# Performance work log

Measured on AMD Instinct MI355X. Metric: run time of the kernel, lower is better.

The kernel has to match this reference:

```python
import jax, jax.numpy as jnp
import numpy as np

N = 64000
B = 16
F_IN = 16
N_PROP = 64
N_DIM = 4
K = 40        # n_neighbours
F_OUT = 128


def setup_inputs() -> dict:
    key = jax.random.key(0)
    ks = jax.random.split(key, 8)
    x = jax.random.normal(ks[0], (N, F_IN), dtype=jnp.float32)
    row_splits = (jnp.arange(B + 1, dtype=jnp.int32) * (N // B))
    # Dense params (glorot-ish scaling)
    Ws = jax.random.normal(ks[1], (F_IN, N_DIM), dtype=jnp.float32) / jnp.sqrt(F_IN)
    bs = jnp.zeros((N_DIM,), dtype=jnp.float32)
    Wf = jax.random.normal(ks[2], (F_IN, N_PROP), dtype=jnp.float32) / jnp.sqrt(F_IN)
    bf = jnp.zeros((N_PROP,), dtype=jnp.float32)
    n_in = F_IN + 2 * N_PROP  # x concat [max, mean]
    Wo = jax.random.normal(ks[3], (n_in, F_OUT), dtype=jnp.float32) / jnp.sqrt(n_in)
    bo = jnp.zeros((F_OUT,), dtype=jnp.float32)
    return {"x": x, "row_splits": row_splits, "Ws": Ws, "bs": bs,
            "Wf": Wf, "bf": bf, "Wo": Wo, "bo": bo}


def _knn_indices(coords, n_per_seg, n_seg, k):
    # coords: [N, D] with equal-size segments of n_per_seg nodes.
    c = coords.reshape(n_seg, n_per_seg, -1)              # [B, n, D]
    nn = jnp.sum(c * c, axis=-1)                          # [B, n]
    d2 = nn[:, :, None] + nn[:, None, :] - 2.0 * jnp.einsum('bnd,bmd->bnm', c, c)
    _, idx_local = jax.lax.top_k(-d2, k + 1)              # sorted by distance, self first
    idx_local = idx_local[:, :, 1:]                       # drop self -> [B, n, K]
    offsets = (jnp.arange(n_seg, dtype=idx_local.dtype) * n_per_seg)[:, None, None]
    return (idx_local + offsets).reshape(n_seg * n_per_seg, k)  # global [N, K]


def reference(x, row_splits, Ws, bs, Wf, bf, Wo, bo):
    n_seg = row_splits.shape[0] - 1
    n_per_seg = x.shape[0] // n_seg

    coords = x @ Ws + bs                                  # [N, D]
    feat = x @ Wf + bf                                    # [N, P]

    idx = _knn_indices(coords, n_per_seg, n_seg, K)       # [N, K]
    simple_distance = coords[:, None, :] - coords[idx]    # [N, K, D]
    rot_distance = jnp.sum(simple_distance ** 2, axis=-1) # [N, K]
    # gauss_of_lin(x) = exp(-|x|)
    weights = jnp.exp(-jnp.abs(rot_distance * 10.0 + 1e-5))[..., None]  # [N, K, 1]

    neighbour_features = feat[idx]                        # [N, K, P] gather
    wnf = neighbour_features * weights
    collected = jnp.concatenate([jnp.max(wnf, axis=1), jnp.mean(wnf, axis=1)], axis=-1)
    features = jnp.concatenate([x, collected], axis=-1)   # [N, F_IN + 2P]
    return jnp.tanh(features @ Wo + bo)                   # [N, F_OUT]
```

## Files before the change

### kernel.cpp

```cpp
#include <hip/hip_runtime.h>
#include <math.h>

#define NTOT   64000
#define NSEG   16
#define SEGSZ  4000
#define KNN    40
#define FIN    16
#define NPROP  64
#define FOUT   128
#define NIN    144


__global__ __launch_bounds__(256)
void k1_proj(const float* __restrict__ x,
             const float* __restrict__ Ws, const float* __restrict__ bs,
             const float* __restrict__ Wf, const float* __restrict__ bf,
             float4* __restrict__ coords, float* __restrict__ nn,
             float* __restrict__ feat, float* __restrict__ features)
{
    __shared__ float sWs[FIN * 4];
    __shared__ float sbs[4];
    __shared__ float sWf[FIN * NPROP];
    __shared__ float sbf[NPROP];
    int t = threadIdx.x;
    if (t < FIN * 4) sWs[t] = Ws[t];
    if (t < 4) sbs[t] = bs[t];
    for (int i = t; i < FIN * NPROP; i += 256) sWf[i] = Wf[i];
    if (t < NPROP) sbf[t] = bf[t];
    __syncthreads();

    int q = blockIdx.x * 256 + t;
    const float4* xv = (const float4*)(x + q * FIN);
    float4 x0 = xv[0], x1 = xv[1], x2 = xv[2], x3 = xv[3];
    float xr[FIN] = {x0.x, x0.y, x0.z, x0.w, x1.x, x1.y, x1.z, x1.w,
                     x2.x, x2.y, x2.z, x2.w, x3.x, x3.y, x3.z, x3.w};

    float c0 = sbs[0], c1 = sbs[1], c2 = sbs[2], c3 = sbs[3];
#pragma unroll
    for (int k = 0; k < FIN; k++) {
        float xk = xr[k];
        c0 += xk * sWs[k * 4 + 0];
        c1 += xk * sWs[k * 4 + 1];
        c2 += xk * sWs[k * 4 + 2];
        c3 += xk * sWs[k * 4 + 3];
    }
    coords[q] = make_float4(c0, c1, c2, c3);
    nn[q] = c0 * c0 + c1 * c1 + c2 * c2 + c3 * c3;

    float4* frow = (float4*)(features + q * NIN);
    frow[0] = x0; frow[1] = x1; frow[2] = x2; frow[3] = x3;

#pragma unroll
    for (int f0 = 0; f0 < NPROP; f0 += 4) {
        float a0 = sbf[f0], a1 = sbf[f0 + 1], a2 = sbf[f0 + 2], a3 = sbf[f0 + 3];
#pragma unroll
        for (int k = 0; k < FIN; k++) {
            float xk = xr[k];
            const float* w = &sWf[k * NPROP + f0];
            a0 += xk * w[0]; a1 += xk * w[1]; a2 += xk * w[2]; a3 += xk * w[3];
        }
        *(float4*)(feat + q * NPROP + f0) = make_float4(a0, a1, a2, a3);
    }
}

#define K2_WPB 4
#define QPW    2

__device__ __forceinline__ void ce(unsigned int& a, unsigned int& b)
{
    unsigned int lo = min(a, b);
    unsigned int hi = max(a, b);
    a = lo; b = hi;
}

__device__ __forceinline__ void batch4(unsigned int (&arr)[4],
                                       unsigned int k0, unsigned int k1,
                                       unsigned int k2, unsigned int k3)
{
    ce(k0, k1); ce(k2, k3); ce(k0, k2); ce(k1, k3); ce(k1, k2);
    arr[0] = min(arr[0], k3);
    arr[1] = min(arr[1], k2);
    arr[2] = min(arr[2], k1);
    arr[3] = min(arr[3], k0);
    ce(arr[0], arr[2]); ce(arr[1], arr[3]); ce(arr[0], arr[1]); ce(arr[2], arr[3]);
}

__global__ __launch_bounds__(256)
void k2_knn_agg(const float4* __restrict__ coords, const float* __restrict__ nn,
                const float* __restrict__ feat, float* __restrict__ features)
{
    __shared__ unsigned int win[K2_WPB][QPW][KNN];
    int lane = threadIdx.x & 63;
    int wave = threadIdx.x >> 6;
    int qA = (blockIdx.x * K2_WPB + wave) * QPW;
    int seg = qA / SEGSZ;
    int segbase = seg * SEGSZ;
    int lqA = qA - segbase;
    float4 qcA = coords[qA];
    float4 qcB = coords[qA + 1];
    const float4* cbase = coords + segbase;
    const float* nbase = nn + segbase;

    float sqqA = qcA.x * qcA.x + qcA.y * qcA.y + qcA.z * qcA.z + qcA.w * qcA.w;
    float sqqB = qcB.x * qcB.x + qcB.y * qcB.y + qcB.z * qcB.z + qcB.w * qcB.w;
    float mAx = -2.f * qcA.x, mAy = -2.f * qcA.y, mAz = -2.f * qcA.z, mAw = -2.f * qcA.w;
    float mBx = -2.f * qcB.x, mBy = -2.f * qcB.y, mBz = -2.f * qcB.z, mBw = -2.f * qcB.w;

    unsigned int arrA[4], arrB[4];
#pragma unroll
    for (int n = 0; n < 4; n++) { arrA[n] = 0xFFFFFFFFu; arrB[n] = 0xFFFFFFFFu; }

#define DKEY(cc, njs, j, mx, my, mz, mw) \
    ((__float_as_uint(fmaxf(fmaf((cc).x, (mx), fmaf((cc).y, (my), \
      fmaf((cc).z, (mz), fmaf((cc).w, (mw), (njs))))), 0.f)) & 0xFFFFF000u) \
     | (unsigned int)(j))

    for (int b = 0; b < 15; b++) {
        int j0 = b * 256 + lane;
        float4 c0 = cbase[j0];
        float4 c1 = cbase[j0 + 64];
        float4 c2 = cbase[j0 + 128];
        float4 c3 = cbase[j0 + 192];
        float n0 = nbase[j0], n1 = nbase[j0 + 64];
        float n2 = nbase[j0 + 128], n3 = nbase[j0 + 192];
        unsigned int a0 = DKEY(c0, n0 + sqqA, j0,       mAx, mAy, mAz, mAw);
        unsigned int a1 = DKEY(c1, n1 + sqqA, j0 + 64,  mAx, mAy, mAz, mAw);
        unsigned int a2 = DKEY(c2, n2 + sqqA, j0 + 128, mAx, mAy, mAz, mAw);
        unsigned int a3 = DKEY(c3, n3 + sqqA, j0 + 192, mAx, mAy, mAz, mAw);
        batch4(arrA, a0, a1, a2, a3);
        unsigned int b0 = DKEY(c0, n0 + sqqB, j0,       mBx, mBy, mBz, mBw);
        unsigned int b1 = DKEY(c1, n1 + sqqB, j0 + 64,  mBx, mBy, mBz, mBw);
        unsigned int b2 = DKEY(c2, n2 + sqqB, j0 + 128, mBx, mBy, mBz, mBw);
        unsigned int b3 = DKEY(c3, n3 + sqqB, j0 + 192, mBx, mBy, mBz, mBw);
        batch4(arrB, b0, b1, b2, b3);
    }
    {
        int j0 = 3840 + lane;
        float4 c0 = cbase[j0];
        float4 c1 = cbase[j0 + 64];
        float n0 = nbase[j0], n1 = nbase[j0 + 64];
        int j2 = j0 + 128;
        int j2c = (j2 < SEGSZ) ? j2 : (SEGSZ - 1);
        float4 c2 = cbase[j2c];
        float n2 = nbase[j2c];
        unsigned int a0 = DKEY(c0, n0 + sqqA, j0,      mAx, mAy, mAz, mAw);
        unsigned int a1 = DKEY(c1, n1 + sqqA, j0 + 64, mAx, mAy, mAz, mAw);
        unsigned int a2 = (j2 < SEGSZ)
            ? (unsigned int)DKEY(c2, n2 + sqqA, j2, mAx, mAy, mAz, mAw)
            : 0xFFFFFFFFu;
        batch4(arrA, a0, a1, a2, 0xFFFFFFFFu);
        unsigned int b0 = DKEY(c0, n0 + sqqB, j0,      mBx, mBy, mBz, mBw);
        unsigned int b1 = DKEY(c1, n1 + sqqB, j0 + 64, mBx, mBy, mBz, mBw);
        unsigned int b2 = (j2 < SEGSZ)
            ? (unsigned int)DKEY(c2, n2 + sqqB, j2, mBx, mBy, mBz, mBw)
            : 0xFFFFFFFFu;
        batch4(arrB, b0, b1, b2, 0xFFFFFFFFu);
    }
#undef DKEY

    const float* fseg = feat + segbase * NPROP + lane;

#define SELECT_AND_AGG(ARR, LQ, Q, SLOT)                                      \
    {                                                                         \
        unsigned int klo = 0u, khi = 0xFFFFFFFFu;                             \
        for (int it = 0; it < 32; it++) {                                     \
            unsigned int mid = klo + ((khi - klo) >> 1);                      \
            int c = 0;                                                        \
            c += __popcll(__ballot(ARR[0] <= mid));                           \
            c += __popcll(__ballot(ARR[1] <= mid));                           \
            c += __popcll(__ballot(ARR[2] <= mid));                           \
            c += __popcll(__ballot(ARR[3] <= mid));                           \
            if (c >= KNN + 1) khi = mid; else klo = mid + 1;                  \
        }                                                                     \
        unsigned int K41 = khi;                                               \
        int base = 0;                                                         \
        _Pragma("unroll")                                                     \
        for (int n = 0; n < 4; n++) {                                         \
            bool qual = (ARR[n] <= K41) &&                                    \
                        ((ARR[n] & 0xFFFu) != (unsigned int)(LQ));            \
            unsigned long long m = __ballot(qual);                            \
            int pos = base + __builtin_amdgcn_mbcnt_hi((unsigned int)(m >> 32),\
                            __builtin_amdgcn_mbcnt_lo((unsigned int)m, 0));   \
            if (qual && pos < KNN) win[wave][SLOT][pos] = ARR[n];             \
            base += __popcll(m);                                              \
            if (base >= KNN) break;                                           \
        }                                                                     \
        float mxv = -INFINITY, smv = 0.f;                                     \
        _Pragma("unroll 4")                                                   \
        for (int k = 0; k < KNN; k++) {                                       \
            unsigned int key = win[wave][SLOT][k];                            \
            float d2 = __uint_as_float(key & 0xFFFFF000u);                    \
            int nl = (int)(key & 0xFFFu);                                     \
            float w = __expf(-(d2 * 10.f + 1e-5f));                           \
            float f = fseg[nl * NPROP];                                       \
            float wf = w * f;                                                 \
            mxv = fmaxf(mxv, wf);                                             \
            smv += wf;                                                        \
        }                                                                     \
        features[(Q) * NIN + FIN + lane]         = mxv;                       \
        features[(Q) * NIN + FIN + NPROP + lane] = smv * (1.f / KNN);         \
    }

    SELECT_AND_AGG(arrA, lqA,     qA,     0)
    SELECT_AND_AGG(arrB, lqA + 1, qA + 1, 1)
#undef SELECT_AND_AGG
}

__global__ __launch_bounds__(256)
void k4_gemm(const float* __restrict__ features, const float* __restrict__ Wo,
             const float* __restrict__ bo, float* __restrict__ out)
{
    __shared__ float As[16 * 128];
    __shared__ float Bs[16 * 128];
    int t = threadIdx.x;
    int ty = t >> 4, tx = t & 15;
    int r0 = blockIdx.x * 128;

    float acc[8][8];
#pragma unroll
    for (int i = 0; i < 8; i++)
#pragma unroll
        for (int j = 0; j < 8; j++) acc[i][j] = 0.f;

    int arow = t >> 1;
    int acol = (t & 1) * 8;

    for (int c = 0; c < 9; c++) {
        const float* asrc = features + (r0 + arow) * NIN + c * 16 + acol;
        float4 a0 = *(const float4*)(asrc);
        float4 a1 = *(const float4*)(asrc + 4);
        const float4* bsrc = (const float4*)(Wo + c * 2048 + t * 8);
        float4 b0 = bsrc[0], b1 = bsrc[1];
        As[(acol + 0) * 128 + arow] = a0.x;
        As[(acol + 1) * 128 + arow] = a0.y;
        As[(acol + 2) * 128 + arow] = a0.z;
        As[(acol + 3) * 128 + arow] = a0.w;
        As[(acol + 4) * 128 + arow] = a1.x;
        As[(acol + 5) * 128 + arow] = a1.y;
        As[(acol + 6) * 128 + arow] = a1.z;
        As[(acol + 7) * 128 + arow] = a1.w;
        *(float4*)&Bs[t * 8]     = b0;
        *(float4*)&Bs[t * 8 + 4] = b1;
        __syncthreads();
#pragma unroll
        for (int kk = 0; kk < 16; kk++) {
            float4 av0 = *(float4*)&As[kk * 128 + ty * 8];
            float4 av1 = *(float4*)&As[kk * 128 + ty * 8 + 4];
            float4 bv0 = *(float4*)&Bs[kk * 128 + tx * 8];
            float4 bv1 = *(float4*)&Bs[kk * 128 + tx * 8 + 4];
            float a[8] = {av0.x, av0.y, av0.z, av0.w, av1.x, av1.y, av1.z, av1.w};
            float b[8] = {bv0.x, bv0.y, bv0.z, bv0.w, bv1.x, bv1.y, bv1.z, bv1.w};
#pragma unroll
            for (int i = 0; i < 8; i++)
#pragma unroll
                for (int j = 0; j < 8; j++) acc[i][j] += a[i] * b[j];
        }
        __syncthreads();
    }

#pragma unroll
    for (int i = 0; i < 8; i++) {
        int r = r0 + ty * 8 + i;
        float4 o0, o1;
        o0.x = tanhf(acc[i][0] + bo[tx * 8 + 0]);
        o0.y = tanhf(acc[i][1] + bo[tx * 8 + 1]);
        o0.z = tanhf(acc[i][2] + bo[tx * 8 + 2]);
        o0.w = tanhf(acc[i][3] + bo[tx * 8 + 3]);
        o1.x = tanhf(acc[i][4] + bo[tx * 8 + 4]);
        o1.y = tanhf(acc[i][5] + bo[tx * 8 + 5]);
        o1.z = tanhf(acc[i][6] + bo[tx * 8 + 6]);
        o1.w = tanhf(acc[i][7] + bo[tx * 8 + 7]);
        *(float4*)(out + r * FOUT + tx * 8)     = o0;
        *(float4*)(out + r * FOUT + tx * 8 + 4) = o1;
    }
}

extern "C" void kernel_launch(void* const* d_in, const int* in_sizes, int n_in,
                              void* d_out, int out_size, void* d_ws, size_t ws_size,
                              hipStream_t stream)
{
    const float* x  = (const float*)d_in[0];
    const float* Ws = (const float*)d_in[2];
    const float* bs = (const float*)d_in[3];
    const float* Wf = (const float*)d_in[4];
    const float* bf = (const float*)d_in[5];
    const float* Wo = (const float*)d_in[6];
    const float* bo = (const float*)d_in[7];
    float* out = (float*)d_out;

    char* ws = (char*)d_ws;
    float4* coords   = (float4*)(ws);
    float*  nn       = (float*)(ws + 1024000);
    float*  feat     = (float*)(ws + 1280000);
    float*  features = (float*)(ws + 17664000);

    hipLaunchKernelGGL(k1_proj,    dim3(250),  dim3(256), 0, stream,
                       x, Ws, bs, Wf, bf, coords, nn, feat, features);
    hipLaunchKernelGGL(k2_knn_agg, dim3(8000), dim3(256), 0, stream,
                       coords, nn, feat, features);
    hipLaunchKernelGGL(k4_gemm,    dim3(500),  dim3(256), 0, stream,
                       features, Wo, bo, out);
}
```

Before: 195.4 us.

## Store features as bf16 and run the output GEMM on bf16 MFMA

The intermediate feature matrix is now written in bf16 by the projection and aggregation kernels instead of fp32. The output GEMM uses __builtin_amdgcn_mfma_f32_16x16x32_bf16 with a transposed, K-padded bf16 copy of Wo staged in LDS, replacing the scalar FMA tiled GEMM. tanh is computed through __expf. This cuts GEMM compute and the memory traffic on the intermediate buffer. In exchange, every block re-converts Wo into LDS, bf16 rounding lowers accuracy, and the K padding from 144 to 160 reads past each row's end.

```diff
diff --git a/kernel.cpp b/kernel.cpp
--- a/kernel.cpp
+++ b/kernel.cpp
@@ -1,4 +1,5 @@
 #include <hip/hip_runtime.h>
+#include <hip/hip_bf16.h>
 #include <math.h>
 
 #define NTOT   64000
@@ -10,13 +11,23 @@
 #define FOUT   128
 #define NIN    144
 
+typedef unsigned short u16;
+typedef __attribute__((ext_vector_type(8))) short bf16x8;
+typedef __attribute__((ext_vector_type(4))) float f32x4;
+
+__device__ __forceinline__ u16 f2bf(float f)
+{
+    __hip_bfloat16 h = __float2bfloat16(f);
+    return *reinterpret_cast<u16*>(&h);
+}
+
 
 __global__ __launch_bounds__(256)
 void k1_proj(const float* __restrict__ x,
              const float* __restrict__ Ws, const float* __restrict__ bs,
              const float* __restrict__ Wf, const float* __restrict__ bf,
              float4* __restrict__ coords, float* __restrict__ nn,
-             float* __restrict__ feat, float* __restrict__ features)
+             float* __restrict__ feat, u16* __restrict__ featB)
 {
     __shared__ float sWs[FIN * 4];
     __shared__ float sbs[4];
@@ -47,8 +58,14 @@
     coords[q] = make_float4(c0, c1, c2, c3);
     nn[q] = c0 * c0 + c1 * c1 + c2 * c2 + c3 * c3;
 
-    float4* frow = (float4*)(features + q * NIN);
-    frow[0] = x0; frow[1] = x1; frow[2] = x2; frow[3] = x3;
+    unsigned int xp[8];
+#pragma unroll
+    for (int i = 0; i < 8; i++)
+        xp[i] = (unsigned int)f2bf(xr[2 * i]) |
+                ((unsigned int)f2bf(xr[2 * i + 1]) << 16);
+    uint4* fb = (uint4*)(featB + (size_t)q * NIN);
+    fb[0] = make_uint4(xp[0], xp[1], xp[2], xp[3]);
+    fb[1] = make_uint4(xp[4], xp[5], xp[6], xp[7]);
 
 #pragma unroll
     for (int f0 = 0; f0 < NPROP; f0 += 4) {
@@ -87,7 +104,7 @@
 
 __global__ __launch_bounds__(256)
 void k2_knn_agg(const float4* __restrict__ coords, const float* __restrict__ nn,
-                const float* __restrict__ feat, float* __restrict__ features)
+                const float* __restrict__ feat, u16* __restrict__ featB)
 {
     __shared__ unsigned int win[K2_WPB][QPW][KNN];
     int lane = threadIdx.x & 63;
@@ -197,8 +214,8 @@
             mxv = fmaxf(mxv, wf);                                             \
             smv += wf;                                                        \
         }                                                                     \
-        features[(Q) * NIN + FIN + lane]         = mxv;                       \
-        features[(Q) * NIN + FIN + NPROP + lane] = smv * (1.f / KNN);         \
+        featB[(size_t)(Q) * NIN + FIN + lane]         = f2bf(mxv);            \
+        featB[(size_t)(Q) * NIN + FIN + NPROP + lane] = f2bf(smv * (1.f/KNN));\
     }
 
     SELECT_AND_AGG(arrA, lqA,     qA,     0)
@@ -207,71 +224,56 @@
 }
 
 __global__ __launch_bounds__(256)
-void k4_gemm(const float* __restrict__ features, const float* __restrict__ Wo,
+void k4_gemm(const u16* __restrict__ featB, const float* __restrict__ Wo,
              const float* __restrict__ bo, float* __restrict__ out)
 {
-    __shared__ float As[16 * 128];
-    __shared__ float Bs[16 * 128];
+    __shared__ u16 BsT[128 * 168];
+
     int t = threadIdx.x;
-    int ty = t >> 4, tx = t & 15;
-    int r0 = blockIdx.x * 128;
-
-    float acc[8][8];
-#pragma unroll
-    for (int i = 0; i < 8; i++)
-#pragma unroll
-        for (int j = 0; j < 8; j++) acc[i][j] = 0.f;
-
-    int arow = t >> 1;
-    int acol = (t & 1) * 8;
-
-    for (int c = 0; c < 9; c++) {
-        const float* asrc = features + (r0 + arow) * NIN + c * 16 + acol;
-        float4 a0 = *(const float4*)(asrc);
-        float4 a1 = *(const float4*)(asrc + 4);
-        const float4* bsrc = (const float4*)(Wo + c * 2048 + t * 8);
-        float4 b0 = bsrc[0], b1 = bsrc[1];
-        As[(acol + 0) * 128 + arow] = a0.x;
-        As[(acol + 1) * 128 + arow] = a0.y;
-        As[(acol + 2) * 128 + arow] = a0.z;
-        As[(acol + 3) * 128 + arow] = a0.w;
-        As[(acol + 4) * 128 + arow] = a1.x;
-        As[(acol + 5) * 128 + arow] = a1.y;
-        As[(acol + 6) * 128 + arow] = a1.z;
-        As[(acol + 7) * 128 + arow] = a1.w;
-        *(float4*)&Bs[t * 8]     = b0;
-        *(float4*)&Bs[t * 8 + 4] = b1;
-        __syncthreads();
-#pragma unroll
-        for (int kk = 0; kk < 16; kk++) {
-            float4 av0 = *(float4*)&As[kk * 128 + ty * 8];
-            float4 av1 = *(float4*)&As[kk * 128 + ty * 8 + 4];
-            float4 bv0 = *(float4*)&Bs[kk * 128 + tx * 8];
-            float4 bv1 = *(float4*)&Bs[kk * 128 + tx * 8 + 4];
-            float a[8] = {av0.x, av0.y, av0.z, av0.w, av1.x, av1.y, av1.z, av1.w};
-            float b[8] = {bv0.x, bv0.y, bv0.z, bv0.w, bv1.x, bv1.y, bv1.z, bv1.w};
-#pragma unroll
-            for (int i = 0; i < 8; i++)
-#pragma unroll
-                for (int j = 0; j < 8; j++) acc[i][j] += a[i] * b[j];
+    for (int idx = t; idx < 80 * 128; idx += 256) {
+        int kp = idx >> 7;
+        int col = idx & 127;
+        int k0 = kp * 2;
+        float w0 = (k0 < NIN)     ? Wo[k0 * FOUT + col]       : 0.f;
+        float w1 = (k0 + 1 < NIN) ? Wo[(k0 + 1) * FOUT + col] : 0.f;
+        unsigned int pk = (unsigned int)f2bf(w0) | ((unsigned int)f2bf(w1) << 16);
+        *(unsigned int*)&BsT[col * 168 + k0] = pk;
+    }
+    __syncthreads();
+
+    int lane = t & 63;
+    int wave = t >> 6;
+    int R = blockIdx.x * 64 + wave * 16;
+    int rc = lane & 15;
+    int koff = lane >> 4;
+
+    f32x4 acc[8];
+#pragma unroll
+    for (int c = 0; c < 8; c++) acc[c] = (f32x4){0.f, 0.f, 0.f, 0.f};
+
+    const u16* arow = featB + (size_t)(R + rc) * NIN + koff * 8;
+#pragma unroll
+    for (int kc = 0; kc < 5; kc++) {
+        bf16x8 af = *(const bf16x8*)(arow + kc * 32);
+#pragma unroll
+        for (int c = 0; c < 8; c++) {
+            const u16* bp = &BsT[(c * 16 + rc) * 168 + kc * 32 + koff * 8];
+            bf16x8 bfr = *(const bf16x8*)bp;
+            acc[c] = __builtin_amdgcn_mfma_f32_16x16x32_bf16(af, bfr, acc[c], 0, 0, 0);
         }
-        __syncthreads();
-    }
-
-#pragma unroll
-    for (int i = 0; i < 8; i++) {
-        int r = r0 + ty * 8 + i;
-        float4 o0, o1;
-        o0.x = tanhf(acc[i][0] + bo[tx * 8 + 0]);
-        o0.y = tanhf(acc[i][1] + bo[tx * 8 + 1]);
-        o0.z = tanhf(acc[i][2] + bo[tx * 8 + 2]);
-        o0.w = tanhf(acc[i][3] + bo[tx * 8 + 3]);
-        o1.x = tanhf(acc[i][4] + bo[tx * 8 + 4]);
-        o1.y = tanhf(acc[i][5] + bo[tx * 8 + 5]);
-        o1.z = tanhf(acc[i][6] + bo[tx * 8 + 6]);
-        o1.w = tanhf(acc[i][7] + bo[tx * 8 + 7]);
-        *(float4*)(out + r * FOUT + tx * 8)     = o0;
-        *(float4*)(out + r * FOUT + tx * 8 + 4) = o1;
+    }
+
+    int orow = R + koff * 4;
+#pragma unroll
+    for (int c = 0; c < 8; c++) {
+        int col = c * 16 + rc;
+        float b = bo[col];
+#pragma unroll
+        for (int r = 0; r < 4; r++) {
+            float z = acc[c][r] + b;
+            float e = __expf(2.f * z);
+            out[(size_t)(orow + r) * FOUT + col] = 1.f - 2.f / (e + 1.f);
+        }
     }
 }
 
@@ -289,15 +291,15 @@
     float* out = (float*)d_out;
 
     char* ws = (char*)d_ws;
-    float4* coords   = (float4*)(ws);
-    float*  nn       = (float*)(ws + 1024000);
-    float*  feat     = (float*)(ws + 1280000);
-    float*  features = (float*)(ws + 17664000);
+    float4* coords = (float4*)(ws);
+    float*  nn     = (float*)(ws + 1024000);
+    float*  feat   = (float*)(ws + 1280000);
+    u16*    featB  = (u16*)(ws + 17664000);
 
     hipLaunchKernelGGL(k1_proj,    dim3(250),  dim3(256), 0, stream,
-                       x, Ws, bs, Wf, bf, coords, nn, feat, features);
+                       x, Ws, bs, Wf, bf, coords, nn, feat, featB);
     hipLaunchKernelGGL(k2_knn_agg, dim3(8000), dim3(256), 0, stream,
-                       coords, nn, feat, features);
-    hipLaunchKernelGGL(k4_gemm,    dim3(500),  dim3(256), 0, stream,
-                       features, Wo, bo, out);
-}
+                       coords, nn, feat, featB);
+    hipLaunchKernelGGL(k4_gemm,    dim3(1000), dim3(256), 0, stream,
+                       featB, Wo, bo, out);
+}
```

After: 203.3 us. +4.1%, slower.
